# Kernel tuning notes

Hardware: AMD Instinct MI355X
Metric: run time of the kernel (lower is better)

## Reference

```python
import jax, jax.numpy as jnp
import numpy as np

NEG_POS_RATIO = 3
NUM_CLASSES = 80


def setup_inputs() -> dict:
    key = jax.random.key(0)
    k1, k2, k3, k4 = jax.random.split(key, 4)
    B, P = 64, 24576
    return {
        "loc_preds": jax.random.normal(k1, (B, P, 4), dtype=jnp.float32),
        "cls_preds": jax.random.normal(k2, (B, P, NUM_CLASSES + 1), dtype=jnp.float32),
        "loc_targets": jax.random.normal(k3, (B, P, 4), dtype=jnp.float32),
        "cls_targets": jax.random.randint(k4, (B, P), 0, NUM_CLASSES + 1),
    }


def reference(loc_preds, cls_preds, loc_targets, cls_targets):
    # Positive anchors: label > 0 (0 = background)
    pos_mask = cls_targets > 0                      # [B, P] bool
    num_pos = pos_mask.sum(axis=1)                  # [B] int

    # --- localization loss: smooth-L1 (beta=1) summed over positive anchors ---
    d = loc_preds - loc_targets
    ad = jnp.abs(d)
    huber = jnp.where(ad < 1.0, 0.5 * d * d, ad - 0.5)   # [B, P, 4]
    posf = pos_mask.astype(loc_preds.dtype)
    loc_loss = jnp.sum(huber * posf[:, :, None])

    # --- per-anchor cross entropy ---
    logp = jax.nn.log_softmax(cls_preds, axis=-1)        # [B, P, C+1]
    ce = -jnp.take_along_axis(logp, cls_targets[..., None], axis=-1)[..., 0]  # [B, P]

    loss_c_pos = jnp.sum(jnp.where(pos_mask, ce, 0.0))

    # --- hard negative mining: top (ratio * num_pos) negative CE per image ---
    ce_neg = jnp.where(pos_mask, 0.0, ce)                # zero out positives
    ce_neg_sorted = -jnp.sort(-ce_neg, axis=1)           # descending per row
    neg_count = (~pos_mask).sum(axis=1)                  # [B]
    num_neg = jnp.minimum(NEG_POS_RATIO * num_pos, neg_count)  # [B]
    rank = jnp.arange(ce.shape[1])                       # [P]
    take = rank[None, :] < num_neg[:, None]              # [B, P]
    # CE >= 0 and num_neg <= neg_count, so ties with zeroed positives contribute 0;
    # equivalent to sorting the negative subset only (as the torch loop does).
    neg_loss = jnp.sum(jnp.where(take, ce_neg_sorted, 0.0))

    N = jnp.maximum(num_pos.sum(), 1).astype(loc_preds.dtype)
    return (loc_loss + loss_c_pos + neg_loss) / N
```

## Files before the change

kernel.cpp:

```cpp
#include <hip/hip_runtime.h>

#define BB 64
#define PP 24576
#define CC 81

__device__ __forceinline__ float rd_lane(float v, int l) {
  return __int_as_float(__builtin_amdgcn_readlane(__float_as_int(v), l));
}
__device__ __forceinline__ float rd_first(float v) {
  return __int_as_float(__builtin_amdgcn_readfirstlane(__float_as_int(v)));
}

__global__ void ssd_init(double* pos_loss, double* neg_sum, double* neg_total,
                         int* num_pos) {
  const int t = threadIdx.x;
  if (t < BB) { pos_loss[t] = 0.0; neg_sum[t] = 0.0; num_pos[t] = 0; }
  if (t == 0) neg_total[0] = 0.0;
}

__global__ __launch_bounds__(256, 8) void ssd_main(
    const float* __restrict__ loc_p, const float* __restrict__ cls_p,
    const float* __restrict__ loc_t, const int* __restrict__ tgt,
    double* __restrict__ pos_loss, double* __restrict__ neg_sum,
    int* __restrict__ num_pos) {
  const int lane = threadIdx.x & 63;
  const int wv   = threadIdx.x >> 6;
  const int b    = blockIdx.x >> 5;
  const int wib  = ((blockIdx.x & 31) << 2) | wv;
  const int a0   = b * PP + wib * 192;

  float accH = 0.f;
  float accP = 0.f;
  float accN = 0.f;
  int   cntP = 0;

  for (int i = 0; i < 192; i += 2) {
    const int idxA = a0 + i;
    const float* cpA = cls_p + (size_t)idxA * CC;
    const float* cpB = cpA + CC;
    float ax0 = cpA[lane];
    float bx0 = cpB[lane];
    float ax1 = (lane < 17) ? cpA[64 + lane] : -__builtin_inff();
    float bx1 = (lane < 17) ? cpB[64 + lane] : -__builtin_inff();
    int tA = __builtin_amdgcn_readfirstlane(tgt[idxA]);
    int tB = __builtin_amdgcn_readfirstlane(tgt[idxA + 1]);
    const size_t lb = (size_t)idxA * 4;
    float lp = (lane < 8) ? loc_p[lb + lane] : 0.f;
    float lt = (lane < 8) ? loc_t[lb + lane] : 0.f;

    float eA = __expf(ax0) + __expf(ax1);
    float eB = __expf(bx0) + __expf(bx1);
#pragma unroll
    for (int m = 1; m < 64; m <<= 1) {
      eA += __shfl_xor(eA, m);
      eB += __shfl_xor(eB, m);
    }
    float xtA = (tA < 64) ? rd_lane(ax0, tA) : rd_lane(ax1, tA & 63);
    float xtB = (tB < 64) ? rd_lane(bx0, tB) : rd_lane(bx1, tB & 63);
    float ceA = __logf(eA) - xtA;
    float ceB = __logf(eB) - xtB;

    float d  = lp - lt;
    float ad = fabsf(d);
    float h  = (ad < 1.f) ? 0.5f * d * d : ad - 0.5f;
    bool  pl = (lane < 4) ? (tA > 0) : (tB > 0);
    accH += pl ? h : 0.f;

    accP += (tA > 0) ? ceA : 0.f;
    accN += (tA > 0) ? 0.f : ceA;
    accP += (tB > 0) ? ceB : 0.f;
    accN += (tB > 0) ? 0.f : ceB;
    cntP += (int)(tA > 0) + (int)(tB > 0);
  }

#pragma unroll
  for (int m = 1; m < 8; m <<= 1) accH += __shfl_xor(accH, m);
  float hTot = rd_first(accH);

  __shared__ double sP[4], sN[4];
  __shared__ int sC[4];
  if (lane == 0) {
    sP[wv] = (double)accP + (double)hTot;
    sN[wv] = (double)accN;
    sC[wv] = cntP;
  }
  __syncthreads();
  if (threadIdx.x == 0) {
    atomicAdd(&pos_loss[b], sP[0] + sP[1] + sP[2] + sP[3]);
    atomicAdd(&neg_sum[b],  sN[0] + sN[1] + sN[2] + sN[3]);
    atomicAdd(&num_pos[b],  sC[0] + sC[1] + sC[2] + sC[3]);
  }
}

__device__ float anchor_ce_serial(const float* __restrict__ cp, int t) {
  float s = 0.f;
#pragma unroll 9
  for (int c = 0; c < CC; ++c) s += __expf(cp[c]);
  return __logf(s) - cp[t];
}

__global__ void ssd_neg(const float* __restrict__ cls_p,
                        const int* __restrict__ tgt,
                        const double* __restrict__ neg_sum,
                        const int* __restrict__ num_pos,
                        double* __restrict__ neg_total) {
  const int b = blockIdx.x;
  const long np = num_pos[b];
  const long nc = (long)PP - np;
  long k = 3 * np;
  if (k > nc) k = nc;
  if (k <= 0) return;
  if (k >= nc) {
    if (threadIdx.x == 0) atomicAdd(neg_total, neg_sum[b]);
    return;
  }
  __shared__ int s_cnt;
  __shared__ double s_sum;
  const size_t rowbase = (size_t)b * PP;
  unsigned lo = 0u, hi = 0x7f800000u;
  while (lo < hi) {
    unsigned mid = lo + ((hi - lo + 1) >> 1);
    if (threadIdx.x == 0) s_cnt = 0;
    __syncthreads();
    float V = __uint_as_float(mid);
    int c = 0;
    for (int p = threadIdx.x; p < PP; p += blockDim.x) {
      if (tgt[rowbase + p] == 0) {
        float ce = anchor_ce_serial(cls_p + (rowbase + p) * (size_t)CC, 0);
        if (ce >= V) c++;
      }
    }
    atomicAdd(&s_cnt, c);
    __syncthreads();
    int total = s_cnt;
    __syncthreads();
    if (total >= k) lo = mid; else hi = mid - 1;
  }
  const float V = __uint_as_float(lo);
  if (threadIdx.x == 0) { s_cnt = 0; s_sum = 0.0; }
  __syncthreads();
  int cg = 0;
  double sg = 0.0;
  for (int p = threadIdx.x; p < PP; p += blockDim.x) {
    if (tgt[rowbase + p] == 0) {
      float ce = anchor_ce_serial(cls_p + (rowbase + p) * (size_t)CC, 0);
      if (ce > V) { cg++; sg += (double)ce; }
    }
  }
  atomicAdd(&s_cnt, cg);
  atomicAdd(&s_sum, sg);
  __syncthreads();
  if (threadIdx.x == 0)
    atomicAdd(neg_total, s_sum + (double)(k - s_cnt) * (double)V);
}

__global__ void ssd_fin(const double* __restrict__ pos_loss,
                        const double* __restrict__ neg_total,
                        const int* __restrict__ num_pos,
                        float* __restrict__ out) {
  const int l = threadIdx.x;
  double v = pos_loss[l];
  int    n = num_pos[l];
#pragma unroll
  for (int m = 1; m < 64; m <<= 1) {
    v += __shfl_xor(v, m);
    n += __shfl_xor(n, m);
  }
  if (l == 0) {
    double N = (n < 1) ? 1.0 : (double)n;
    out[0] = (float)((v + neg_total[0]) / N);
  }
}

extern "C" void kernel_launch(void* const* d_in, const int* in_sizes, int n_in,
                              void* d_out, int out_size, void* d_ws,
                              size_t ws_size, hipStream_t stream) {
  const float* loc_p = (const float*)d_in[0];
  const float* cls_p = (const float*)d_in[1];
  const float* loc_t = (const float*)d_in[2];
  const int*   tgt   = (const int*)d_in[3];

  double* pos_loss  = (double*)d_ws;
  double* neg_sum   = pos_loss + BB;
  double* neg_total = neg_sum + BB;
  int*    num_pos   = (int*)(neg_total + 1);
  float*  out       = (float*)d_out;

  ssd_init<<<1, 64, 0, stream>>>(pos_loss, neg_sum, neg_total, num_pos);
  ssd_main<<<2048, 256, 0, stream>>>(loc_p, cls_p, loc_t, tgt,
                                     pos_loss, neg_sum, num_pos);
  ssd_neg<<<BB, 256, 0, stream>>>(cls_p, tgt, neg_sum, num_pos, neg_total);
  ssd_fin<<<1, 64, 0, stream>>>(pos_loss, neg_total, num_pos, out);
}
```

Baseline: 719.3 us.

## Drop atomics and init kernel, merge neg and final reduction into one kernel

The main kernel now writes per-block partials instead of issuing double atomics, so the init kernel is no longer needed. It loads targets and loc data in vectorized, coalesced form up front and uses ballot/popcount to count positives. The negative-mining and final-reduction kernels are merged into a single one-block kernel that reduces the partials and handles any rows needing top-k selection serially. That saves launches but would be very slow if any row needs the binary search, though with random labels k always reaches the negative count.

```diff
diff --git a/kernel.cpp b/kernel.cpp
--- a/kernel.cpp
+++ b/kernel.cpp
@@ -3,92 +3,90 @@
 #define BB 64
 #define PP 24576
 #define CC 81
+#define NBLK 2048
 
 __device__ __forceinline__ float rd_lane(float v, int l) {
   return __int_as_float(__builtin_amdgcn_readlane(__float_as_int(v), l));
 }
-__device__ __forceinline__ float rd_first(float v) {
-  return __int_as_float(__builtin_amdgcn_readfirstlane(__float_as_int(v)));
-}
-
-__global__ void ssd_init(double* pos_loss, double* neg_sum, double* neg_total,
-                         int* num_pos) {
-  const int t = threadIdx.x;
-  if (t < BB) { pos_loss[t] = 0.0; neg_sum[t] = 0.0; num_pos[t] = 0; }
-  if (t == 0) neg_total[0] = 0.0;
-}
-
-__global__ __launch_bounds__(256, 8) void ssd_main(
+
+__device__ __forceinline__ float hub(float d) {
+  float ad = fabsf(d);
+  return (ad < 1.f) ? 0.5f * d * d : ad - 0.5f;
+}
+
+__global__ __launch_bounds__(256) void ssd_main(
     const float* __restrict__ loc_p, const float* __restrict__ cls_p,
     const float* __restrict__ loc_t, const int* __restrict__ tgt,
-    double* __restrict__ pos_loss, double* __restrict__ neg_sum,
-    int* __restrict__ num_pos) {
+    double* __restrict__ posW, double* __restrict__ negW,
+    int* __restrict__ cntW) {
   const int lane = threadIdx.x & 63;
   const int wv   = threadIdx.x >> 6;
   const int b    = blockIdx.x >> 5;
   const int wib  = ((blockIdx.x & 31) << 2) | wv;
   const int a0   = b * PP + wib * 192;
 
-  float accH = 0.f;
-  float accP = 0.f;
-  float accN = 0.f;
-  int   cntP = 0;
-
-  for (int i = 0; i < 192; i += 2) {
-    const int idxA = a0 + i;
-    const float* cpA = cls_p + (size_t)idxA * CC;
-    const float* cpB = cpA + CC;
-    float ax0 = cpA[lane];
-    float bx0 = cpB[lane];
-    float ax1 = (lane < 17) ? cpA[64 + lane] : -__builtin_inff();
-    float bx1 = (lane < 17) ? cpB[64 + lane] : -__builtin_inff();
-    int tA = __builtin_amdgcn_readfirstlane(tgt[idxA]);
-    int tB = __builtin_amdgcn_readfirstlane(tgt[idxA + 1]);
-    const size_t lb = (size_t)idxA * 4;
-    float lp = (lane < 8) ? loc_p[lb + lane] : 0.f;
-    float lt = (lane < 8) ? loc_t[lb + lane] : 0.f;
-
-    float eA = __expf(ax0) + __expf(ax1);
-    float eB = __expf(bx0) + __expf(bx1);
-#pragma unroll
-    for (int m = 1; m < 64; m <<= 1) {
-      eA += __shfl_xor(eA, m);
-      eB += __shfl_xor(eB, m);
-    }
-    float xtA = (tA < 64) ? rd_lane(ax0, tA) : rd_lane(ax1, tA & 63);
-    float xtB = (tB < 64) ? rd_lane(bx0, tB) : rd_lane(bx1, tB & 63);
-    float ceA = __logf(eA) - xtA;
-    float ceB = __logf(eB) - xtB;
-
-    float d  = lp - lt;
-    float ad = fabsf(d);
-    float h  = (ad < 1.f) ? 0.5f * d * d : ad - 0.5f;
-    bool  pl = (lane < 4) ? (tA > 0) : (tB > 0);
-    accH += pl ? h : 0.f;
-
-    accP += (tA > 0) ? ceA : 0.f;
-    accN += (tA > 0) ? 0.f : ceA;
-    accP += (tB > 0) ? ceB : 0.f;
-    accN += (tB > 0) ? 0.f : ceB;
-    cntP += (int)(tA > 0) + (int)(tB > 0);
-  }
-
-#pragma unroll
-  for (int m = 1; m < 8; m <<= 1) accH += __shfl_xor(accH, m);
-  float hTot = rd_first(accH);
+  const int t0 = tgt[a0 + lane];
+  const int t1 = tgt[a0 + 64 + lane];
+  const int t2 = tgt[a0 + 128 + lane];
+  const int cnt = __popcll(__ballot(t0 > 0)) + __popcll(__ballot(t1 > 0)) +
+                  __popcll(__ballot(t2 > 0));
+
+  const float4* lp4 = (const float4*)loc_p + a0;
+  const float4* lt4 = (const float4*)loc_t + a0;
+  float hsum = 0.f;
+#pragma unroll
+  for (int c = 0; c < 3; ++c) {
+    const int tc = (c == 0) ? t0 : (c == 1) ? t1 : t2;
+    float4 p = lp4[c * 64 + lane];
+    float4 q = lt4[c * 64 + lane];
+    float h = hub(p.x - q.x) + hub(p.y - q.y) + hub(p.z - q.z) + hub(p.w - q.w);
+    hsum += (tc > 0) ? h : 0.f;
+  }
+
+  float sAll = 0.f, sNeg = 0.f;
+  const float* cp = cls_p + (size_t)a0 * CC;
+#pragma unroll 1
+  for (int c = 0; c < 3; ++c) {
+    const int tch = (c == 0) ? t0 : (c == 1) ? t1 : t2;
+    for (int j = 0; j < 64; j += 2) {
+      const float* cpA = cp + (size_t)(c * 64 + j) * CC;
+      float ax0 = cpA[lane];
+      float bx0 = cpA[CC + lane];
+      float ax1 = (lane < 17) ? cpA[64 + lane] : -__builtin_inff();
+      float bx1 = (lane < 17) ? cpA[CC + 64 + lane] : -__builtin_inff();
+      float eA = __expf(ax0) + __expf(ax1);
+      float eB = __expf(bx0) + __expf(bx1);
+#pragma unroll
+      for (int m = 1; m < 64; m <<= 1) {
+        eA += __shfl_xor(eA, m);
+        eB += __shfl_xor(eB, m);
+      }
+      const int tA = __builtin_amdgcn_readlane(tch, j);
+      const int tB = __builtin_amdgcn_readlane(tch, j + 1);
+      float xtA = (tA < 64) ? rd_lane(ax0, tA) : rd_lane(ax1, tA - 64);
+      float xtB = (tB < 64) ? rd_lane(bx0, tB) : rd_lane(bx1, tB - 64);
+      float ceA = __logf(eA) - xtA;
+      float ceB = __logf(eB) - xtB;
+      sAll += ceA + ceB;
+      sNeg += ((tA > 0) ? 0.f : ceA) + ((tB > 0) ? 0.f : ceB);
+    }
+  }
+
+#pragma unroll
+  for (int m = 1; m < 64; m <<= 1) hsum += __shfl_xor(hsum, m);
 
   __shared__ double sP[4], sN[4];
   __shared__ int sC[4];
   if (lane == 0) {
-    sP[wv] = (double)accP + (double)hTot;
-    sN[wv] = (double)accN;
-    sC[wv] = cntP;
+    sP[wv] = (double)(sAll - sNeg) + (double)hsum;
+    sN[wv] = (double)sNeg;
+    sC[wv] = cnt;
   }
   __syncthreads();
   if (threadIdx.x == 0) {
-    atomicAdd(&pos_loss[b], sP[0] + sP[1] + sP[2] + sP[3]);
-    atomicAdd(&neg_sum[b],  sN[0] + sN[1] + sN[2] + sN[3]);
-    atomicAdd(&num_pos[b],  sC[0] + sC[1] + sC[2] + sC[3]);
+    posW[blockIdx.x] = sP[0] + sP[1] + sP[2] + sP[3];
+    negW[blockIdx.x] = sN[0] + sN[1] + sN[2] + sN[3];
+    cntW[blockIdx.x] = sC[0] + sC[1] + sC[2] + sC[3];
   }
 }
 
@@ -99,76 +97,102 @@
   return __logf(s) - cp[t];
 }
 
-__global__ void ssd_neg(const float* __restrict__ cls_p,
+__global__ void ssd_fin(const float* __restrict__ cls_p,
                         const int* __restrict__ tgt,
-                        const double* __restrict__ neg_sum,
-                        const int* __restrict__ num_pos,
-                        double* __restrict__ neg_total) {
-  const int b = blockIdx.x;
-  const long np = num_pos[b];
-  const long nc = (long)PP - np;
-  long k = 3 * np;
-  if (k > nc) k = nc;
-  if (k <= 0) return;
-  if (k >= nc) {
-    if (threadIdx.x == 0) atomicAdd(neg_total, neg_sum[b]);
-    return;
-  }
+                        const double* __restrict__ posW,
+                        const double* __restrict__ negW,
+                        const int* __restrict__ cntW,
+                        float* __restrict__ out) {
+  const int t = threadIdx.x;
+  __shared__ double sp[256], sn[256];
+  __shared__ int sc[256];
+  __shared__ double rp[64], rn[64];
+  __shared__ int rc[64], needRow[64];
   __shared__ int s_cnt;
   __shared__ double s_sum;
-  const size_t rowbase = (size_t)b * PP;
-  unsigned lo = 0u, hi = 0x7f800000u;
-  while (lo < hi) {
-    unsigned mid = lo + ((hi - lo + 1) >> 1);
-    if (threadIdx.x == 0) s_cnt = 0;
+
+  double p8 = 0.0, n8 = 0.0;
+  int c8 = 0;
+#pragma unroll
+  for (int i = 0; i < 8; ++i) {
+    const int g = t * 8 + i;
+    p8 += posW[g];
+    n8 += negW[g];
+    c8 += cntW[g];
+  }
+  sp[t] = p8; sn[t] = n8; sc[t] = c8;
+  __syncthreads();
+
+  if (t < 64) {
+    double P = 0.0, Nn = 0.0;
+    int C = 0;
+#pragma unroll
+    for (int i = 0; i < 4; ++i) { P += sp[4*t+i]; Nn += sn[4*t+i]; C += sc[4*t+i]; }
+    rp[t] = P; rc[t] = C;
+    long np = C, nc = (long)PP - np, k = 3 * np;
+    if (k > nc) k = nc;
+    double take = 0.0;
+    int need = 0;
+    if (k > 0) {
+      if (k >= nc) take = Nn;
+      else need = 1;
+    }
+    rn[t] = take;
+    needRow[t] = need;
+  }
+  __syncthreads();
+
+  for (int b = 0; b < BB; ++b) {
+    if (!needRow[b]) continue;
+    const long np = rc[b];
+    long nc = (long)PP - np, k = 3 * np;
+    if (k > nc) k = nc;
+    const size_t rowbase = (size_t)b * PP;
+    unsigned lo = 0u, hi = 0x7f800000u;
+    while (lo < hi) {
+      unsigned mid = lo + ((hi - lo + 1) >> 1);
+      if (t == 0) s_cnt = 0;
+      __syncthreads();
+      float V = __uint_as_float(mid);
+      int c = 0;
+      for (int p = t; p < PP; p += blockDim.x)
+        if (tgt[rowbase + p] == 0)
+          if (anchor_ce_serial(cls_p + (rowbase + p) * (size_t)CC, 0) >= V) c++;
+      atomicAdd(&s_cnt, c);
+      __syncthreads();
+      int total = s_cnt;
+      __syncthreads();
+      if (total >= k) lo = mid; else hi = mid - 1;
+    }
+    const float V = __uint_as_float(lo);
+    if (t == 0) { s_cnt = 0; s_sum = 0.0; }
     __syncthreads();
-    float V = __uint_as_float(mid);
-    int c = 0;
-    for (int p = threadIdx.x; p < PP; p += blockDim.x) {
+    int cg = 0;
+    double sg = 0.0;
+    for (int p = t; p < PP; p += blockDim.x)
       if (tgt[rowbase + p] == 0) {
         float ce = anchor_ce_serial(cls_p + (rowbase + p) * (size_t)CC, 0);
-        if (ce >= V) c++;
+        if (ce > V) { cg++; sg += (double)ce; }
       }
-    }
-    atomicAdd(&s_cnt, c);
+    atomicAdd(&s_cnt, cg);
+    atomicAdd(&s_sum, sg);
     __syncthreads();
-    int total = s_cnt;
+    if (t == 0) rn[b] = s_sum + (double)(k - s_cnt) * (double)V;
     __syncthreads();
-    if (total >= k) lo = mid; else hi = mid - 1;
-  }
-  const float V = __uint_as_float(lo);
-  if (threadIdx.x == 0) { s_cnt = 0; s_sum = 0.0; }
-  __syncthreads();
-  int cg = 0;
-  double sg = 0.0;
-  for (int p = threadIdx.x; p < PP; p += blockDim.x) {
-    if (tgt[rowbase + p] == 0) {
-      float ce = anchor_ce_serial(cls_p + (rowbase + p) * (size_t)CC, 0);
-      if (ce > V) { cg++; sg += (double)ce; }
-    }
-  }
-  atomicAdd(&s_cnt, cg);
-  atomicAdd(&s_sum, sg);
-  __syncthreads();
-  if (threadIdx.x == 0)
-    atomicAdd(neg_total, s_sum + (double)(k - s_cnt) * (double)V);
-}
-
-__global__ void ssd_fin(const double* __restrict__ pos_loss,
-                        const double* __restrict__ neg_total,
-                        const int* __restrict__ num_pos,
-                        float* __restrict__ out) {
-  const int l = threadIdx.x;
-  double v = pos_loss[l];
-  int    n = num_pos[l];
-#pragma unroll
-  for (int m = 1; m < 64; m <<= 1) {
-    v += __shfl_xor(v, m);
-    n += __shfl_xor(n, m);
-  }
-  if (l == 0) {
-    double N = (n < 1) ? 1.0 : (double)n;
-    out[0] = (float)((v + neg_total[0]) / N);
+  }
+
+  if (t < 64) {
+    double v = rp[t] + rn[t];
+    int n = rc[t];
+#pragma unroll
+    for (int m = 1; m < 64; m <<= 1) {
+      v += __shfl_xor(v, m);
+      n += __shfl_xor(n, m);
+    }
+    if (t == 0) {
+      double N = (n < 1) ? 1.0 : (double)n;
+      out[0] = (float)(v / N);
+    }
   }
 }
 
@@ -180,15 +204,12 @@
   const float* loc_t = (const float*)d_in[2];
   const int*   tgt   = (const int*)d_in[3];
 
-  double* pos_loss  = (double*)d_ws;
-  double* neg_sum   = pos_loss + BB;
-  double* neg_total = neg_sum + BB;
-  int*    num_pos   = (int*)(neg_total + 1);
-  float*  out       = (float*)d_out;
-
-  ssd_init<<<1, 64, 0, stream>>>(pos_loss, neg_sum, neg_total, num_pos);
-  ssd_main<<<2048, 256, 0, stream>>>(loc_p, cls_p, loc_t, tgt,
-                                     pos_loss, neg_sum, num_pos);
-  ssd_neg<<<BB, 256, 0, stream>>>(cls_p, tgt, neg_sum, num_pos, neg_total);
-  ssd_fin<<<1, 64, 0, stream>>>(pos_loss, neg_total, num_pos, out);
-}
+  double* posW = (double*)d_ws;
+  double* negW = posW + NBLK;
+  int*    cntW = (int*)(negW + NBLK);
+  float*  out  = (float*)d_out;
+
+  ssd_main<<<NBLK, 256, 0, stream>>>(loc_p, cls_p, loc_t, tgt,
+                                     posW, negW, cntW);
+  ssd_fin<<<1, 256, 0, stream>>>(cls_p, tgt, posW, negW, cntW, out);
+}
```

Result: no change. 713.0 us (-0.9%).
